# Performance work log

Measured on AMD Instinct MI355X. Metric: run time of the kernel, lower is better.

## Reference

```python
import jax, jax.numpy as jnp
import numpy as np

EPS_LN = 1e-5
EPS_STD = 1e-5


def _ln_dim1(z, g, b):
    # LayerNorm over channel dim (axis=1) of (B, C, T) or (B, C, 1)
    mu = z.mean(axis=1, keepdims=True)
    var = ((z - mu) ** 2).mean(axis=1, keepdims=True)
    return (z - mu) * jax.lax.rsqrt(var + EPS_LN) * g[None, :, None] + b[None, :, None]


def _stats(x, m):
    # weighted mean/std over time axis; m broadcasts over channels
    mean = (m * x).sum(axis=2)                                   # (B, C)
    std = jnp.sqrt(jnp.maximum((m * x * x).sum(axis=2) - mean ** 2, EPS_STD))
    return mean, std


def setup_inputs() -> dict:
    key = jax.random.key(0)
    ks = jax.random.split(key, 4)
    B, C, T, H = 16, 1536, 2000, 128
    x = jax.random.normal(ks[0], (B, C, T), dtype=jnp.float32)
    mask = jnp.ones((B, 1, T), dtype=jnp.float32)
    # attention MLP params (conv1x1 -> relu -> LN(dim=1) -> tanh -> conv1x1)
    w1 = jax.random.normal(ks[1], (H, 3 * C), dtype=jnp.float32) * (1.0 / np.sqrt(3 * C))
    b1 = jnp.zeros((H,), jnp.float32)
    g1 = jnp.ones((H,), jnp.float32)
    be1 = jnp.zeros((H,), jnp.float32)
    w2 = jax.random.normal(ks[2], (C, H), dtype=jnp.float32) * (1.0 / np.sqrt(H))
    b2 = jnp.zeros((C,), jnp.float32)
    g2 = jnp.ones((2 * C,), jnp.float32)
    be2 = jnp.zeros((2 * C,), jnp.float32)
    return {"x": x, "mask": mask, "w1": w1, "b1": b1, "g1": g1, "be1": be1,
            "w2": w2, "b2": b2, "g2": g2, "be2": be2}


def reference(x, mask, w1, b1, g1, be1, w2, b2, g2, be2):
    B, C, T = x.shape
    # time_attention: append masked global mean/std, broadcast over T
    total = mask.sum(axis=2, keepdims=True)                      # (B,1,1)
    mean0, std0 = _stats(x, mask / total)                        # (B,C)
    x_in = jnp.concatenate([
        x,
        jnp.broadcast_to(mean0[:, :, None], (B, C, T)),
        jnp.broadcast_to(std0[:, :, None], (B, C, T)),
    ], axis=1)                                                   # (B,3C,T)
    # attention MLP (conv1x1 == channel matmul)
    h = jnp.einsum("hc,bct->bht", w1, x_in) + b1[None, :, None]  # (B,H,T)
    h = jnp.tanh(_ln_dim1(jax.nn.relu(h), g1, be1))
    alpha = jnp.einsum("ch,bht->bct", w2, h) + b2[None, :, None]  # (B,C,T)
    # masked softmax over time
    alpha = jnp.where(mask == 0, -jnp.inf, alpha)
    alpha = jax.nn.softmax(alpha, axis=2)
    # attention-weighted stats
    mean, std = _stats(x, alpha)                                 # (B,C) each
    out = jnp.concatenate([mean, std], axis=1)[:, :, None]       # (B,2C,1)
    return _ln_dim1(out, g2, be2)
```

## Files before the change

kernel.cpp:

```cpp
#include <hip/hip_runtime.h>
#include <hip/hip_bf16.h>
#include <math.h>

constexpr int B_  = 16;
constexpr int C_  = 1536;
constexpr int T_  = 2000;
constexpr int H_  = 128;
constexpr int C3_ = 3 * C_;
constexpr int C2_ = 2 * C_;
constexpr int NT_ = 4;

typedef short bf8 __attribute__((ext_vector_type(8)));
typedef short bf4 __attribute__((ext_vector_type(4)));
typedef float f4  __attribute__((ext_vector_type(4)));

__device__ inline unsigned short f2b(float f) {
  __bf16 h = (__bf16)f;
  return __builtin_bit_cast(unsigned short, h);
}

__global__ __launch_bounds__(256) void k_stats(
    const float* __restrict__ x, const float* __restrict__ mask,
    float* __restrict__ mean0, float* __restrict__ std0) {
  const int wave = threadIdx.x >> 6;
  const int lane = threadIdx.x & 63;
  const int row = blockIdx.x * 4 + wave;
  const int b = row / C_;
  const float4* xr = (const float4*)(x + (size_t)row * T_);
  const float4* mr = (const float4*)(mask + (size_t)b * T_);
  float sm = 0.f, s1 = 0.f, s2 = 0.f;
  for (int i = lane; i < T_ / 4; i += 64) {
    float4 xv = xr[i];
    float4 mv = mr[i];
    sm += mv.x + mv.y + mv.z + mv.w;
    s1 += mv.x * xv.x + mv.y * xv.y + mv.z * xv.z + mv.w * xv.w;
    s2 += mv.x * xv.x * xv.x + mv.y * xv.y * xv.y + mv.z * xv.z * xv.z + mv.w * xv.w * xv.w;
  }
#pragma unroll
  for (int off = 32; off; off >>= 1) {
    sm += __shfl_xor(sm, off);
    s1 += __shfl_xor(s1, off);
    s2 += __shfl_xor(s2, off);
  }
  if (lane == 0) {
    float mean = s1 / sm;
    float var = s2 / sm - mean * mean;
    mean0[row] = mean;
    std0[row] = sqrtf(fmaxf(var, 1e-5f));
  }
}

__global__ __launch_bounds__(256) void k_hconst_wl1(
    const float* __restrict__ w1, const float* __restrict__ b1,
    const float* __restrict__ mean0, const float* __restrict__ std0,
    const float* __restrict__ w2,
    float* __restrict__ hconst, float* __restrict__ wl1) {
  const int wave = threadIdx.x >> 6;
  const int lane = threadIdx.x & 63;
  if (blockIdx.x < B_ * H_ / 4) {
    const int idx = blockIdx.x * 4 + wave;
    const int b = idx >> 7;
    const int h = idx & (H_ - 1);
    const float* wm  = w1 + (size_t)h * C3_ + C_;
    const float* wsd = wm + C_;
    const float* mn = mean0 + b * C_;
    const float* sd = std0 + b * C_;
    float s = 0.f;
    for (int c = lane; c < C_; c += 64)
      s += wm[c] * mn[c] + wsd[c] * sd[c];
#pragma unroll
    for (int off = 32; off; off >>= 1) s += __shfl_xor(s, off);
    if (lane == 0) hconst[idx] = s + b1[h];
  } else {
    const int c = (blockIdx.x - B_ * H_ / 4) * 4 + wave;
    const float* wr = w2 + (size_t)c * H_;
    float s = fabsf(wr[lane]) + fabsf(wr[lane + 64]);
#pragma unroll
    for (int off = 32; off; off >>= 1) s += __shfl_xor(s, off);
    if (lane == 0) wl1[c] = s;
  }
}

__global__ __launch_bounds__(256) void k_gemm1_ln(
    const float* __restrict__ x, const float* __restrict__ w1,
    const float* __restrict__ hconst, const float* __restrict__ g1,
    const float* __restrict__ be1, unsigned short* __restrict__ hlnT) {
  __shared__ __align__(16) short As[2][128 * 32];
  const int b = blockIdx.y;
  const int t0 = blockIdx.x * 64;
  const int tid = threadIdx.x;
  const int lane = tid & 63;
  const int w = tid >> 6;
  const int l15 = lane & 15;
  const int l4 = lane >> 4;
  const int tcl = min(t0 + w * 16 + l15, T_ - 1);
  const float* xcol = x + (size_t)b * C_ * T_ + tcl;

  float4 va[4];
  float xs0[8], xs1[8];

  f4 acc[8];
#pragma unroll
  for (int mi = 0; mi < 8; ++mi) { f4 z = {0.f, 0.f, 0.f, 0.f}; acc[mi] = z; }

#define G1_GLOADA(K0)                                                         \
  {                                                                           \
    _Pragma("unroll")                                                         \
    for (int q = 0; q < 4; ++q) {                                             \
      int idx = q * 256 + tid;                                                \
      int row = idx >> 3, j4 = idx & 7;                                       \
      va[q] = *(const float4*)(w1 + (size_t)row * C3_ + (K0) + j4 * 4);       \
    }                                                                         \
  }
#define G1_GLOADB(K0, XS)                                                     \
  {                                                                           \
    const float* xb = xcol + ((size_t)(K0) + l4 * 8) * T_;                    \
    _Pragma("unroll")                                                         \
    for (int j = 0; j < 8; ++j) XS[j] = xb[(size_t)j * T_];                   \
  }
#define G1_LSTOREA(BUF)                                                       \
  {                                                                           \
    _Pragma("unroll")                                                         \
    for (int q = 0; q < 4; ++q) {                                             \
      int idx = q * 256 + tid;                                                \
      int row = idx >> 3, j4 = idx & 7;                                       \
      int slot = (j4 >> 1) ^ ((row >> 2) & 3);                                \
      bf4 p;                                                                  \
      p[0] = (short)f2b(va[q].x); p[1] = (short)f2b(va[q].y);                 \
      p[2] = (short)f2b(va[q].z); p[3] = (short)f2b(va[q].w);                 \
      *(bf4*)&As[BUF][row * 32 + slot * 8 + (j4 & 1) * 4] = p;                \
    }                                                                         \
  }
#define G1_STEP(S, XSCUR, XSNXT, CUR)                                         \
  {                                                                           \
    if ((S) + 1 < NS) {                                                       \
      G1_GLOADA(((S) + 1) * 32);                                              \
      G1_GLOADB(((S) + 1) * 32, XSNXT);                                       \
    }                                                                         \
    bf8 bfr;                                                                  \
    _Pragma("unroll")                                                         \
    for (int j = 0; j < 8; ++j) bfr[j] = (short)f2b(XSCUR[j]);                \
    _Pragma("unroll")                                                         \
    for (int mi = 0; mi < 8; ++mi) {                                          \
      bf8 afr = *(const bf8*)&As[CUR][(mi * 16 + l15) * 32 + (l4 ^ fA) * 8];  \
      acc[mi] = __builtin_amdgcn_mfma_f32_16x16x32_bf16(afr, bfr, acc[mi], 0, 0, 0); \
    }                                                                         \
    if ((S) + 1 < NS) G1_LSTOREA(CUR ^ 1);                                    \
    __syncthreads();                                                          \
  }

  const int fA = (l15 >> 2) & 3;
  const int NS = C_ / 32;

  G1_GLOADA(0);
  G1_GLOADB(0, xs0);
  G1_LSTOREA(0);
  __syncthreads();

  for (int sp = 0; sp < NS / 2; ++sp) {
    G1_STEP(2 * sp,     xs0, xs1, 0);
    G1_STEP(2 * sp + 1, xs1, xs0, 1);
  }

  const int t = t0 + w * 16 + l15;
  float sum = 0.f, ssq = 0.f;
#pragma unroll
  for (int mi = 0; mi < 8; ++mi) {
    float4 h4 = *(const float4*)(hconst + b * H_ + mi * 16 + l4 * 4);
    const float* hp = (const float*)&h4;
#pragma unroll
    for (int reg = 0; reg < 4; ++reg) {
      float v = fmaxf(acc[mi][reg] + hp[reg], 0.f);
      acc[mi][reg] = v;
      sum += v;
      ssq += v * v;
    }
  }
  sum += __shfl_xor(sum, 16); sum += __shfl_xor(sum, 32);
  ssq += __shfl_xor(ssq, 16); ssq += __shfl_xor(ssq, 32);
  const float mean = sum * (1.f / 128.f);
  const float rstd = rsqrtf(ssq * (1.f / 128.f) - mean * mean + 1e-5f);
  if (t < T_) {
    unsigned short* dst = hlnT + ((size_t)b * T_ + t) * H_;
#pragma unroll
    for (int mi = 0; mi < 8; ++mi) {
      float4 g4 = *(const float4*)(g1 + mi * 16 + l4 * 4);
      float4 e4 = *(const float4*)(be1 + mi * 16 + l4 * 4);
      const float* gp = (const float*)&g4;
      const float* ep = (const float*)&e4;
      bf4 p;
#pragma unroll
      for (int reg = 0; reg < 4; ++reg) {
        float o = tanhf((acc[mi][reg] - mean) * rstd * gp[reg] + ep[reg]);
        p[reg] = (short)f2b(o);
      }
      *(bf4*)&dst[mi * 16 + l4 * 4] = p;
    }
  }
}

__global__ __launch_bounds__(256) void k_gemm2_pool(
    const float* __restrict__ x, const float* __restrict__ mask,
    const float* __restrict__ w2, const unsigned short* __restrict__ hlnT,
    const float* __restrict__ wl1,
    float* __restrict__ ps0, float* __restrict__ ps1, float* __restrict__ ps2) {
  __shared__ __align__(16) short Hs[2][64 * 128];
  const int b = blockIdx.y;
  const int c0 = blockIdx.x * 64;
  const int part = blockIdx.z;
  const int tb = part * 512;
  const int te = min(tb + 512, T_);
  const int tid = threadIdx.x;
  const int lane = tid & 63;
  const int w = tid >> 6;
  const int l15 = lane & 15;
  const int l4 = lane >> 4;

  bf8 af[4];
#pragma unroll
  for (int ks = 0; ks < 4; ++ks) {
    const float* src = w2 + (size_t)(c0 + w * 16 + l15) * H_ + (ks * 4 + l4) * 8;
    float4 v0 = *(const float4*)src;
    float4 v1 = *(const float4*)(src + 4);
    bf8 p;
    p[0] = (short)f2b(v0.x); p[1] = (short)f2b(v0.y);
    p[2] = (short)f2b(v0.z); p[3] = (short)f2b(v0.w);
    p[4] = (short)f2b(v1.x); p[5] = (short)f2b(v1.y);
    p[6] = (short)f2b(v1.z); p[7] = (short)f2b(v1.w);
    af[ks] = p;
  }

  float Mc[4];
  {
    float4 m4 = *(const float4*)(wl1 + c0 + w * 16 + l4 * 4);
    Mc[0] = m4.x; Mc[1] = m4.y; Mc[2] = m4.z; Mc[3] = m4.w;
  }

  float s0[4], s1[4], s2[4];
#pragma unroll
  for (int r = 0; r < 4; ++r) { s0[r] = 0.f; s1[r] = 0.f; s2[r] = 0.f; }

  bf8 hreg[4];
#define G2_HLOAD(T0)                                                          \
  {                                                                           \
    _Pragma("unroll")                                                         \
    for (int q = 0; q < 4; ++q) {                                             \
      int idx = q * 256 + tid;                                                \
      int row = idx >> 4, slot = idx & 15;                                    \
      int t = (T0) + row;                                                     \
      if (t > T_ - 1) t = T_ - 1;                                             \
      hreg[q] = *(const bf8*)(hlnT + ((size_t)b * T_ + t) * H_ + slot * 8);   \
    }                                                                         \
  }
#define G2_HSTORE(BUF)                                                        \
  {                                                                           \
    _Pragma("unroll")                                                         \
    for (int q = 0; q < 4; ++q) {                                             \
      int idx = q * 256 + tid;                                                \
      int row = idx >> 4, slot = idx & 15;                                    \
      *(bf8*)&Hs[BUF][row * 128 + (slot ^ (row & 15)) * 8] = hreg[q];         \
    }                                                                         \
  }

  G2_HLOAD(tb);
  G2_HSTORE(0);
  __syncthreads();

  const int NCH = (te - tb + 63) / 64;
  for (int ch = 0; ch < NCH; ++ch) {
    const int t0 = tb + ch * 64;
    const int cur = ch & 1;
    if (ch + 1 < NCH) G2_HLOAD(t0 + 64);

    float mk[4];
    int tcol[4];
#pragma unroll
    for (int nj = 0; nj < 4; ++nj) {
      int t = t0 + nj * 16 + l15;
      tcol[nj] = (t < T_) ? t : (T_ - 1);
      mk[nj] = (t < T_) ? mask[(size_t)b * T_ + t] : 0.f;
    }
    float xv[4][4];
#pragma unroll
    for (int reg = 0; reg < 4; ++reg) {
      const int c = c0 + w * 16 + l4 * 4 + reg;
      const float* xrow = x + ((size_t)(b * C_ + c)) * T_;
#pragma unroll
      for (int nj = 0; nj < 4; ++nj) xv[reg][nj] = xrow[tcol[nj]];
    }

    f4 acc[4];
#pragma unroll
    for (int nj = 0; nj < 4; ++nj) { f4 z = {0.f, 0.f, 0.f, 0.f}; acc[nj] = z; }

#pragma unroll
    for (int ks = 0; ks < 4; ++ks) {
      const int sw = (ks * 4 + l4) ^ l15;
      bf8 bb[4];
#pragma unroll
      for (int nj = 0; nj < 4; ++nj)
        bb[nj] = *(const bf8*)&Hs[cur][(nj * 16 + l15) * 128 + sw * 8];
#pragma unroll
      for (int nj = 0; nj < 4; ++nj)
        acc[nj] = __builtin_amdgcn_mfma_f32_16x16x32_bf16(af[ks], bb[nj], acc[nj], 0, 0, 0);
    }

#pragma unroll
    for (int reg = 0; reg < 4; ++reg) {
      float a0 = s0[reg], a1 = s1[reg], a2 = s2[reg];
#pragma unroll
      for (int nj = 0; nj < 4; ++nj) {
        float e = (mk[nj] != 0.f) ? __expf(acc[nj][reg] - Mc[reg]) : 0.f;
        float xvv = xv[reg][nj];
        a0 += e; a1 += e * xvv; a2 += e * xvv * xvv;
      }
      s0[reg] = a0; s1[reg] = a1; s2[reg] = a2;
    }

    if (ch + 1 < NCH) G2_HSTORE(cur ^ 1);
    __syncthreads();
  }

#pragma unroll
  for (int off = 1; off < 16; off <<= 1) {
#pragma unroll
    for (int r = 0; r < 4; ++r) {
      s0[r] += __shfl_xor(s0[r], off);
      s1[r] += __shfl_xor(s1[r], off);
      s2[r] += __shfl_xor(s2[r], off);
    }
  }
  if (l15 == 0) {
#pragma unroll
    for (int reg = 0; reg < 4; ++reg) {
      const int c = c0 + w * 16 + l4 * 4 + reg;
      const size_t j = ((size_t)(b * NT_ + part)) * C_ + c;
      ps0[j] = s0[reg]; ps1[j] = s1[reg]; ps2[j] = s2[reg];
    }
  }
}

__global__ __launch_bounds__(256) void k_pool_merge(
    const float* __restrict__ ps0, const float* __restrict__ ps1,
    const float* __restrict__ ps2, float* __restrict__ pooled) {
  const int idx = blockIdx.x * 256 + threadIdx.x;
  const int b = idx / C_;
  const int c = idx - b * C_;
  float s0 = 0.f, s1 = 0.f, s2 = 0.f;
#pragma unroll
  for (int p = 0; p < NT_; ++p) {
    const size_t j = ((size_t)(b * NT_ + p)) * C_ + c;
    s0 += ps0[j]; s1 += ps1[j]; s2 += ps2[j];
  }
  float mean = s1 / s0;
  float var = s2 / s0 - mean * mean;
  pooled[b * C2_ + c] = mean;
  pooled[b * C2_ + C_ + c] = sqrtf(fmaxf(var, 1e-5f));
}

__global__ __launch_bounds__(256) void k_final_ln(
    const float* __restrict__ pooled, const float* __restrict__ g2,
    const float* __restrict__ be2, float* __restrict__ out) {
  __shared__ float rs[8];
  const int b = blockIdx.x;
  const int tid = threadIdx.x;
  const int lane = tid & 63;
  const int wave = tid >> 6;
  const float* p = pooled + b * C2_;
  float s = 0.f, q = 0.f;
  for (int i = tid; i < C2_; i += 256) {
    float v = p[i];
    s += v;
    q += v * v;
  }
#pragma unroll
  for (int off = 32; off; off >>= 1) {
    s += __shfl_xor(s, off);
    q += __shfl_xor(q, off);
  }
  if (lane == 0) { rs[wave] = s; rs[4 + wave] = q; }
  __syncthreads();
  s = rs[0] + rs[1] + rs[2] + rs[3];
  q = rs[4] + rs[5] + rs[6] + rs[7];
  float mean = s * (1.f / C2_);
  float var = q * (1.f / C2_) - mean * mean;
  float rstd = rsqrtf(var + 1e-5f);
  for (int i = tid; i < C2_; i += 256)
    out[b * C2_ + i] = (p[i] - mean) * rstd * g2[i] + be2[i];
}

extern "C" void kernel_launch(void* const* d_in, const int* in_sizes, int n_in,
                              void* d_out, int out_size, void* d_ws, size_t ws_size,
                              hipStream_t stream) {
  const float* x    = (const float*)d_in[0];
  const float* mask = (const float*)d_in[1];
  const float* w1   = (const float*)d_in[2];
  const float* b1   = (const float*)d_in[3];
  const float* g1   = (const float*)d_in[4];
  const float* be1  = (const float*)d_in[5];
  const float* w2   = (const float*)d_in[6];
  const float* g2   = (const float*)d_in[8];
  const float* be2  = (const float*)d_in[9];
  float* out = (float*)d_out;

  float* ws     = (float*)d_ws;
  float* mean0  = ws;
  float* std0   = mean0 + B_ * C_;
  float* hconst = std0 + B_ * C_;
  float* pooled = hconst + B_ * H_;
  float* wl1    = pooled + B_ * C2_;
  float* ps0    = wl1 + C_;
  float* ps1    = ps0 + B_ * NT_ * C_;
  float* ps2    = ps1 + B_ * NT_ * C_;
  unsigned short* hlnT = (unsigned short*)(ps2 + B_ * NT_ * C_);

  k_stats<<<dim3(B_ * C_ / 4), dim3(256), 0, stream>>>(x, mask, mean0, std0);
  k_hconst_wl1<<<dim3(B_ * H_ / 4 + C_ / 4), dim3(256), 0, stream>>>(
      w1, b1, mean0, std0, w2, hconst, wl1);
  k_gemm1_ln<<<dim3((T_ + 63) / 64, B_), dim3(256), 0, stream>>>(x, w1, hconst, g1, be1, hlnT);
  k_gemm2_pool<<<dim3(C_ / 64, B_, NT_), dim3(256), 0, stream>>>(x, mask, w2, hlnT, wl1,
                                                                 ps0, ps1, ps2);
  k_pool_merge<<<dim3(B_ * C_ / 256), dim3(256), 0, stream>>>(ps0, ps1, ps2, pooled);
  k_final_ln<<<dim3(B_), dim3(256), 0, stream>>>(pooled, g2, be2, out);
}
```

Measured before the change: 150.1 us.

## Load GEMM2 B-operand directly from global and fuse pool merge with final LN

The attention-logit GEMM kernel no longer stages the bf16 hidden activations through a double-buffered LDS tile with block barriers. Each wave now reads its MFMA B fragments straight from global/L2, which drops the LDS traffic and the syncthreads at the cost of redundant global loads across the four waves. Separately, the partial-sum merge and the final LayerNorm are fused into one per-batch kernel, which removes one launch and the pooled intermediate buffer.

```diff
diff --git a/kernel.cpp b/kernel.cpp
--- a/kernel.cpp
+++ b/kernel.cpp
@@ -204,7 +204,6 @@
     const float* __restrict__ w2, const unsigned short* __restrict__ hlnT,
     const float* __restrict__ wl1,
     float* __restrict__ ps0, float* __restrict__ ps1, float* __restrict__ ps2) {
-  __shared__ __align__(16) short Hs[2][64 * 128];
   const int b = blockIdx.y;
   const int c0 = blockIdx.x * 64;
   const int part = blockIdx.z;
@@ -240,46 +239,26 @@
 #pragma unroll
   for (int r = 0; r < 4; ++r) { s0[r] = 0.f; s1[r] = 0.f; s2[r] = 0.f; }
 
-  bf8 hreg[4];
-#define G2_HLOAD(T0)                                                          \
-  {                                                                           \
-    _Pragma("unroll")                                                         \
-    for (int q = 0; q < 4; ++q) {                                             \
-      int idx = q * 256 + tid;                                                \
-      int row = idx >> 4, slot = idx & 15;                                    \
-      int t = (T0) + row;                                                     \
-      if (t > T_ - 1) t = T_ - 1;                                             \
-      hreg[q] = *(const bf8*)(hlnT + ((size_t)b * T_ + t) * H_ + slot * 8);   \
-    }                                                                         \
-  }
-#define G2_HSTORE(BUF)                                                        \
-  {                                                                           \
-    _Pragma("unroll")                                                         \
-    for (int q = 0; q < 4; ++q) {                                             \
-      int idx = q * 256 + tid;                                                \
-      int row = idx >> 4, slot = idx & 15;                                    \
-      *(bf8*)&Hs[BUF][row * 128 + (slot ^ (row & 15)) * 8] = hreg[q];         \
-    }                                                                         \
-  }
-
-  G2_HLOAD(tb);
-  G2_HSTORE(0);
-  __syncthreads();
-
-  const int NCH = (te - tb + 63) / 64;
-  for (int ch = 0; ch < NCH; ++ch) {
-    const int t0 = tb + ch * 64;
-    const int cur = ch & 1;
-    if (ch + 1 < NCH) G2_HLOAD(t0 + 64);
-
+  const unsigned short* hb = hlnT + (size_t)b * T_ * H_;
+  const int hoff = l4 * 8;
+
+  for (int t0 = tb; t0 < te; t0 += 64) {
+    int tcol[4];
     float mk[4];
-    int tcol[4];
 #pragma unroll
     for (int nj = 0; nj < 4; ++nj) {
       int t = t0 + nj * 16 + l15;
       tcol[nj] = (t < T_) ? t : (T_ - 1);
       mk[nj] = (t < T_) ? mask[(size_t)b * T_ + t] : 0.f;
     }
+    bf8 bb[4][4];
+#pragma unroll
+    for (int nj = 0; nj < 4; ++nj) {
+      const unsigned short* hp = hb + (size_t)tcol[nj] * H_ + hoff;
+#pragma unroll
+      for (int ks = 0; ks < 4; ++ks)
+        bb[ks][nj] = *(const bf8*)(hp + ks * 32);
+    }
     float xv[4][4];
 #pragma unroll
     for (int reg = 0; reg < 4; ++reg) {
@@ -292,18 +271,11 @@
     f4 acc[4];
 #pragma unroll
     for (int nj = 0; nj < 4; ++nj) { f4 z = {0.f, 0.f, 0.f, 0.f}; acc[nj] = z; }
-
-#pragma unroll
-    for (int ks = 0; ks < 4; ++ks) {
-      const int sw = (ks * 4 + l4) ^ l15;
-      bf8 bb[4];
+#pragma unroll
+    for (int ks = 0; ks < 4; ++ks)
 #pragma unroll
       for (int nj = 0; nj < 4; ++nj)
-        bb[nj] = *(const bf8*)&Hs[cur][(nj * 16 + l15) * 128 + sw * 8];
-#pragma unroll
-      for (int nj = 0; nj < 4; ++nj)
-        acc[nj] = __builtin_amdgcn_mfma_f32_16x16x32_bf16(af[ks], bb[nj], acc[nj], 0, 0, 0);
-    }
+        acc[nj] = __builtin_amdgcn_mfma_f32_16x16x32_bf16(af[ks], bb[ks][nj], acc[nj], 0, 0, 0);
 
 #pragma unroll
     for (int reg = 0; reg < 4; ++reg) {
@@ -316,9 +288,6 @@
       }
       s0[reg] = a0; s1[reg] = a1; s2[reg] = a2;
     }
-
-    if (ch + 1 < NCH) G2_HSTORE(cur ^ 1);
-    __syncthreads();
   }
 
 #pragma unroll
@@ -340,38 +309,32 @@
   }
 }
 
-__global__ __launch_bounds__(256) void k_pool_merge(
+__global__ __launch_bounds__(256) void k_pool_ln(
     const float* __restrict__ ps0, const float* __restrict__ ps1,
-    const float* __restrict__ ps2, float* __restrict__ pooled) {
-  const int idx = blockIdx.x * 256 + threadIdx.x;
-  const int b = idx / C_;
-  const int c = idx - b * C_;
-  float s0 = 0.f, s1 = 0.f, s2 = 0.f;
-#pragma unroll
-  for (int p = 0; p < NT_; ++p) {
-    const size_t j = ((size_t)(b * NT_ + p)) * C_ + c;
-    s0 += ps0[j]; s1 += ps1[j]; s2 += ps2[j];
-  }
-  float mean = s1 / s0;
-  float var = s2 / s0 - mean * mean;
-  pooled[b * C2_ + c] = mean;
-  pooled[b * C2_ + C_ + c] = sqrtf(fmaxf(var, 1e-5f));
-}
-
-__global__ __launch_bounds__(256) void k_final_ln(
-    const float* __restrict__ pooled, const float* __restrict__ g2,
+    const float* __restrict__ ps2, const float* __restrict__ g2,
     const float* __restrict__ be2, float* __restrict__ out) {
   __shared__ float rs[8];
   const int b = blockIdx.x;
   const int tid = threadIdx.x;
   const int lane = tid & 63;
   const int wave = tid >> 6;
-  const float* p = pooled + b * C2_;
+  float mv[6], sv[6];
   float s = 0.f, q = 0.f;
-  for (int i = tid; i < C2_; i += 256) {
-    float v = p[i];
-    s += v;
-    q += v * v;
+#pragma unroll
+  for (int i = 0; i < 6; ++i) {
+    const int c = i * 256 + tid;
+    float a0 = 0.f, a1 = 0.f, a2 = 0.f;
+#pragma unroll
+    for (int p = 0; p < NT_; ++p) {
+      const size_t j = ((size_t)(b * NT_ + p)) * C_ + c;
+      a0 += ps0[j]; a1 += ps1[j]; a2 += ps2[j];
+    }
+    float mean = a1 / a0;
+    float var = a2 / a0 - mean * mean;
+    float sd = sqrtf(fmaxf(var, 1e-5f));
+    mv[i] = mean; sv[i] = sd;
+    s += mean + sd;
+    q += mean * mean + sd * sd;
   }
 #pragma unroll
   for (int off = 32; off; off >>= 1) {
@@ -382,11 +345,15 @@
   __syncthreads();
   s = rs[0] + rs[1] + rs[2] + rs[3];
   q = rs[4] + rs[5] + rs[6] + rs[7];
-  float mean = s * (1.f / C2_);
-  float var = q * (1.f / C2_) - mean * mean;
-  float rstd = rsqrtf(var + 1e-5f);
-  for (int i = tid; i < C2_; i += 256)
-    out[b * C2_ + i] = (p[i] - mean) * rstd * g2[i] + be2[i];
+  const float mu = s * (1.f / C2_);
+  const float var = q * (1.f / C2_) - mu * mu;
+  const float rstd = rsqrtf(var + 1e-5f);
+#pragma unroll
+  for (int i = 0; i < 6; ++i) {
+    const int c = i * 256 + tid;
+    out[b * C2_ + c]      = (mv[i] - mu) * rstd * g2[c] + be2[c];
+    out[b * C2_ + C_ + c] = (sv[i] - mu) * rstd * g2[C_ + c] + be2[C_ + c];
+  }
 }
 
 extern "C" void kernel_launch(void* const* d_in, const int* in_sizes, int n_in,
@@ -407,8 +374,7 @@
   float* mean0  = ws;
   float* std0   = mean0 + B_ * C_;
   float* hconst = std0 + B_ * C_;
-  float* pooled = hconst + B_ * H_;
-  float* wl1    = pooled + B_ * C2_;
+  float* wl1    = hconst + B_ * H_;
   float* ps0    = wl1 + C_;
   float* ps1    = ps0 + B_ * NT_ * C_;
   float* ps2    = ps1 + B_ * NT_ * C_;
@@ -420,6 +386,5 @@
   k_gemm1_ln<<<dim3((T_ + 63) / 64, B_), dim3(256), 0, stream>>>(x, w1, hconst, g1, be1, hlnT);
   k_gemm2_pool<<<dim3(C_ / 64, B_, NT_), dim3(256), 0, stream>>>(x, mask, w2, hlnT, wl1,
                                                                  ps0, ps1, ps2);
-  k_pool_merge<<<dim3(B_ * C_ / 256), dim3(256), 0, stream>>>(ps0, ps1, ps2, pooled);
-  k_final_ln<<<dim3(B_), dim3(256), 0, stream>>>(pooled, g2, be2, out);
-}
+  k_pool_ln<<<dim3(B_), dim3(256), 0, stream>>>(ps0, ps1, ps2, g2, be2, out);
+}
```

Result: slower. 192.8 us (+28.5%).
